# Kernel tuning notes

Measured on AMD Instinct MI355X. Metric: run time of the kernel, lower is better.

The kernel has to match this reference:

```python
import jax, jax.numpy as jnp
import numpy as np

EMBED_DIM = 256
NUM_HEADS = 4
HEAD_DIM = EMBED_DIM // NUM_HEADS  # 64
FEAT_X = FEAT_Y = 64               # 64*64 = 4096 tokens
THETA = 10000.0


def _axial_cos_sin(dim, end_x, end_y, theta):
    # compute_axial_cis: dim//4 frequencies per spatial axis, concatenated -> [N, dim//2]
    f = 1.0 / (theta ** (np.arange(0, dim, 4)[: dim // 4].astype(np.float32) / dim))
    t = np.arange(end_x * end_y)
    tx = (t % end_x).astype(np.float32)
    ty = (t // end_x).astype(np.float32)
    ang = np.concatenate([np.outer(tx, f), np.outer(ty, f)], axis=-1)  # [N, dim//2]
    return jnp.asarray(np.cos(ang)), jnp.asarray(np.sin(ang))


def _apply_rope(x, cos, sin):
    # x: [B, H, N, D]; adjacent pairs (x[..., 2i], x[..., 2i+1]) are the complex parts
    xr = x.reshape(*x.shape[:-1], -1, 2)
    xa, xb = xr[..., 0], xr[..., 1]          # [B, H, N, D//2]
    oa = xa * cos - xb * sin                  # cos/sin: [N, D//2], broadcast
    ob = xa * sin + xb * cos
    return jnp.stack([oa, ob], axis=-1).reshape(x.shape)


def setup_inputs() -> dict:
    key = jax.random.key(0)
    ks = jax.random.split(key, 8)
    B, N, D = 1, FEAT_X * FEAT_Y, EMBED_DIM
    s = 0.02  # weight init scale
    return {
        "q": jax.random.normal(ks[0], (B, N, D), jnp.float32),
        "k": jax.random.normal(ks[1], (B, N, D), jnp.float32),
        "v": jax.random.normal(ks[2], (B, N, D), jnp.float32),
        "wq": jax.random.normal(ks[3], (D, D), jnp.float32) * s,
        "bq": jnp.zeros((D,), jnp.float32),
        "wk": jax.random.normal(ks[4], (D, D), jnp.float32) * s,
        "bk": jnp.zeros((D,), jnp.float32),
        "wv": jax.random.normal(ks[5], (D, D), jnp.float32) * s,
        "bv": jnp.zeros((D,), jnp.float32),
        "wo": jax.random.normal(ks[6], (D, D), jnp.float32) * s,
        "bo": jnp.zeros((D,), jnp.float32),
        "return_attn": 0,
        "num_k_exclude_rope": 0,
    }


def reference(q, k, v, wq, bq, wk, bk, wv, bv, wo, bo, return_attn, num_k_exclude_rope):
    B, Nq, D = q.shape
    H, hd = NUM_HEADS, HEAD_DIM
    # QKV projections (weights stored [in, out], equiv to torch Linear W.T)
    qp = (q @ wq + bq).reshape(B, Nq, H, hd).transpose(0, 2, 1, 3)   # [B,H,Nq,hd]
    kp = (k @ wk + bk).reshape(B, -1, H, hd).transpose(0, 2, 1, 3)   # [B,H,Nk,hd]
    vp = (v @ wv + bv).reshape(B, -1, H, hd).transpose(0, 2, 1, 3)
    # rotary encoding on q and the first (Nk - num_k_exclude_rope) keys
    cos, sin = _axial_cos_sin(hd, FEAT_X, FEAT_Y, THETA)
    qp = _apply_rope(qp, cos, sin)
    nkr = kp.shape[2] - num_k_exclude_rope  # static Python int
    if num_k_exclude_rope > 0:
        kp = jnp.concatenate([_apply_rope(kp[:, :, :nkr], cos, sin), kp[:, :, nkr:]], axis=2)
    else:
        kp = _apply_rope(kp, cos, sin)
    # SDPA (eval: dropout_p = 0)
    scale = 1.0 / jnp.sqrt(jnp.asarray(hd, qp.dtype))
    scores = jnp.einsum("bhqd,bhkd->bhqk", qp, kp) * scale
    attn = jax.nn.softmax(scores, axis=-1)
    out = jnp.einsum("bhqk,bhkd->bhqd", attn, vp)
    out = out.transpose(0, 2, 1, 3).reshape(B, Nq, D)
    out = out @ wo + bo
    if return_attn:
        return out, scores  # attn_weight = q @ k^T * scale (pre-softmax, as in source)
    return out
```

## Files before the change

### kernel.cpp

```cpp
#include <hip/hip_runtime.h>
#include <hip/hip_bf16.h>
#include <math.h>

#define NTOK 4096
#define DEMB 256
#define NHEAD 4
#define HD 64

typedef short bf16x8 __attribute__((ext_vector_type(8)));
typedef short bf16x4 __attribute__((ext_vector_type(4)));
typedef float f32x4 __attribute__((ext_vector_type(4)));

__device__ __forceinline__ unsigned short f2b(float f) {
  union { float f; unsigned u; } v; v.f = f;
  return (unsigned short)((v.u + 0x7FFFu + ((v.u >> 16) & 1u)) >> 16);
}
__device__ __forceinline__ unsigned packrtn(float lo, float hi) {
  union { float f; unsigned u; } a, b; a.f = lo; b.f = hi;
  return ((a.u + 0x8000u) >> 16) | ((b.u + 0x8000u) & 0xFFFF0000u);
}

__global__ void wtrans_kernel(const float* wq, const float* wk, const float* wv,
                              const float* wo, unsigned short* wt) {
  int idx = blockIdx.x * 256 + threadIdx.x;
  int m = idx >> 16, rest = idx & 0xFFFF;
  int o = rest >> 8, i = rest & 255;
  const float* w = (m == 0) ? wq : (m == 1) ? wk : (m == 2) ? wv : wo;
  wt[idx] = f2b(w[i * 256 + o]);
}

__global__ void cs_kernel(float2* cs) {
  int idx = blockIdx.x * 256 + threadIdx.x;
  int n = idx >> 5, p = idx & 31;
  int j = p & 15;
  float f = powf(10000.0f, -(float)j / 16.0f);
  float ang = ((p < 16) ? (float)(n & 63) : (float)(n >> 6)) * f;
  cs[idx] = make_float2(cosf(ang), sinf(ang));
}

__global__ __launch_bounds__(256) void qkvproj_kernel(
    const float* q, const float* k, const float* v, const unsigned short* wt,
    const float* bq, const float* bk, const float* bv, const float2* cs,
    unsigned short* qp, unsigned short* kp, unsigned short* vt) {
  int which = blockIdx.z;
  int wave = threadIdx.x >> 6, lane = threadIdx.x & 63;
  int col = lane & 15, g = lane >> 4;
  int mbase = blockIdx.x * 64 + wave * 16;
  int nbase = blockIdx.y * 64;
  const float* X = (which == 0) ? q : (which == 1) ? k : v;
  const unsigned short* W = wt + which * 65536;
  const float* bias = (which == 0) ? bq : (which == 1) ? bk : bv;

  f32x4 acc[4] = {};
  const float* ap0 = X + (mbase + col) * 256 + g * 8;
#pragma unroll
  for (int ks = 0; ks < 256; ks += 32) {
    float4 a0 = *(const float4*)(ap0 + ks);
    float4 a1 = *(const float4*)(ap0 + ks + 4);
    bf16x8 af;
    af[0] = (short)f2b(a0.x); af[1] = (short)f2b(a0.y);
    af[2] = (short)f2b(a0.z); af[3] = (short)f2b(a0.w);
    af[4] = (short)f2b(a1.x); af[5] = (short)f2b(a1.y);
    af[6] = (short)f2b(a1.z); af[7] = (short)f2b(a1.w);
#pragma unroll
    for (int nt = 0; nt < 4; ++nt) {
      bf16x8 bf_ = *(const bf16x8*)(W + (nbase + nt * 16 + col) * 256 + ks + g * 8);
      acc[nt] = __builtin_amdgcn_mfma_f32_16x16x32_bf16(af, bf_, acc[nt], 0, 0, 0);
    }
  }

  if (which == 2) {
    int kpos = ((mbase >> 5) << 5) + 8 * g + 4 * ((mbase >> 4) & 1);
#pragma unroll
    for (int nt = 0; nt < 4; ++nt) {
      int c = nbase + nt * 16 + col;
      float b = bias[c];
      bf16x4 pk;
#pragma unroll
      for (int r = 0; r < 4; ++r) pk[r] = (short)f2b(acc[nt][r] + b);
      *(bf16x4*)(vt + c * NTOK + kpos) = pk;
    }
  } else {
    const float QSC = 0.18033688f;
    unsigned short* dst = (which == 0) ? qp : kp;
#pragma unroll
    for (int nt = 0; nt < 4; ++nt) {
      int c = nbase + nt * 16 + col;
      float b = bias[c];
#pragma unroll
      for (int r = 0; r < 4; ++r) {
        int t = mbase + g * 4 + r;
        float val = acc[nt][r] + b;
        float2 csv = cs[t * 32 + ((c & 63) >> 1)];
        float pv = __shfl_xor(val, 1);
        float sn = (c & 1) ? csv.y : -csv.y;
        val = val * csv.x + pv * sn;
        if (which == 0) val *= QSC;
        dst[((c >> 6) * NTOK + t) * HD + (c & 63)] = f2b(val);
      }
    }
  }
}

__global__ __launch_bounds__(512, 4) void attn_kernel(
    const unsigned short* qp, const unsigned short* kp,
    const unsigned short* vt, float* pO, float* pml) {
  __shared__ alignas(16) unsigned char lds[32768];
  int id = blockIdx.x;
  int xcd = id & 7;
  int head = xcd >> 1;
  int rest = id >> 3;
  int qtile = rest >> 1;
  int ks = (xcd & 1) * 2 + (rest & 1);
  int qb = qtile * 128;
  int slot = (head * 32 + qtile) * 4 + ks;
  int w = threadIdx.x >> 6, lane = threadIdx.x & 63;
  int col = lane & 15, g = lane >> 4;
  int stok = threadIdx.x >> 3, spart = threadIdx.x & 7;
  unsigned soff = (unsigned)(stok * 128) +
                  (unsigned)((spart * 16) ^ ((stok & 7) << 4));

  const unsigned short* kgp = kp + (head * NTOK + ks * 1024) * HD;
  const unsigned short* vgp = vt + head * HD * NTOK + ks * 1024;

  bf16x8 skr, svr;
  auto stage_issue = [&](int t) {
    skr = *(const bf16x8*)(kgp + (t * 64 + stok) * HD + spart * 8);
    svr = *(const bf16x8*)(vgp + stok * NTOK + t * 64 + spart * 8);
  };
  auto stage_write = [&](int buf) {
    *(bf16x8*)(lds + (unsigned)buf * 16384u + soff) = skr;
    *(bf16x8*)(lds + (unsigned)buf * 16384u + 8192u + soff) = svr;
  };

  bf16x8 qf[2];
  {
    const unsigned short* qr = qp + (head * NTOK + qb + w * 16) * HD;
#pragma unroll
    for (int h2 = 0; h2 < 2; ++h2)
      qf[h2] = *(const bf16x8*)(qr + col * HD + h2 * 32 + g * 8);
  }

  stage_issue(0);
  stage_write(0);
  stage_issue(1);
  __syncthreads();

  f32x4 acco[4] = {};
  float mrow = -1e30f, lrow = 0.f;

  for (int t = 0; t < 16; ++t) {
    int cur = t & 1;
    if (t < 15) {
      stage_write(cur ^ 1);
      if (t < 14) stage_issue(t + 2);
    }
    unsigned kb = (unsigned)cur * 16384u, vb = (unsigned)cur * 16384u + 8192u;

    f32x4 st[4] = {};
#pragma unroll
    for (int mt = 0; mt < 4; ++mt) {
      int tok = mt * 16 + col;
      unsigned ro = kb + (unsigned)(tok * 128) + (unsigned)((g * 16) ^ ((tok & 7) << 4));
      bf16x8 kf0 = *(const bf16x8*)(lds + ro);
      bf16x8 kf1 = *(const bf16x8*)(lds + (ro ^ 64u));
      st[mt] = __builtin_amdgcn_mfma_f32_16x16x32_bf16(kf0, qf[0], st[mt], 0, 0, 0);
      st[mt] = __builtin_amdgcn_mfma_f32_16x16x32_bf16(kf1, qf[1], st[mt], 0, 0, 0);
    }

    float pm = fmaxf(fmaxf(st[0][0], st[0][1]), fmaxf(st[0][2], st[0][3]));
#pragma unroll
    for (int mt = 1; mt < 4; ++mt)
      pm = fmaxf(pm, fmaxf(fmaxf(st[mt][0], st[mt][1]), fmaxf(st[mt][2], st[mt][3])));
    if (!__all(pm <= mrow + 8.0f)) {
      float nm = fmaxf(pm, __shfl_xor(pm, 16));
      nm = fmaxf(nm, __shfl_xor(nm, 32));
      nm = fmaxf(nm, mrow);
      float fac = exp2f(mrow - nm);
      mrow = nm;
      lrow *= fac;
      float fr0 = __shfl(fac, g * 4 + 0), fr1 = __shfl(fac, g * 4 + 1);
      float fr2 = __shfl(fac, g * 4 + 2), fr3 = __shfl(fac, g * 4 + 3);
#pragma unroll
      for (int nt = 0; nt < 4; ++nt) {
        acco[nt][0] *= fr0; acco[nt][1] *= fr1;
        acco[nt][2] *= fr2; acco[nt][3] *= fr3;
      }
    }

    float p[4][4];
#pragma unroll
    for (int mt = 0; mt < 4; ++mt)
#pragma unroll
      for (int r = 0; r < 4; ++r) {
        p[mt][r] = exp2f(st[mt][r] - mrow);
        lrow += p[mt][r];
      }
    unsigned pw[2][4];
#pragma unroll
    for (int kk = 0; kk < 2; ++kk) {
      pw[kk][0] = packrtn(p[2 * kk][0], p[2 * kk][1]);
      pw[kk][1] = packrtn(p[2 * kk][2], p[2 * kk][3]);
      pw[kk][2] = packrtn(p[2 * kk + 1][0], p[2 * kk + 1][1]);
      pw[kk][3] = packrtn(p[2 * kk + 1][2], p[2 * kk + 1][3]);
    }

#pragma unroll
    for (int kk = 0; kk < 2; ++kk) {
      union { unsigned u[4]; bf16x8 v; } pf;
      pf.u[0] = pw[kk][0]; pf.u[1] = pw[kk][1];
      pf.u[2] = pw[kk][2]; pf.u[3] = pw[kk][3];
#pragma unroll
      for (int nt = 0; nt < 4; ++nt) {
        int d = nt * 16 + col;
        unsigned off = vb + (unsigned)(d * 128) +
                       (unsigned)((kk * 64 + g * 16) ^ ((d & 7) << 4));
        bf16x8 vf = *(const bf16x8*)(lds + off);
        acco[nt] = __builtin_amdgcn_mfma_f32_16x16x32_bf16(pf.v, vf, acco[nt], 0, 0, 0);
      }
    }
    __syncthreads();
  }

  lrow += __shfl_xor(lrow, 16);
  lrow += __shfl_xor(lrow, 32);

#pragma unroll
  for (int nt = 0; nt < 4; ++nt)
#pragma unroll
    for (int r = 0; r < 4; ++r)
      pO[slot * 8192 + (w * 16 + g * 4 + r) * 64 + nt * 16 + col] = acco[nt][r];
  if (g == 0) {
    pml[slot * 256 + (w * 16 + col) * 2 + 0] = mrow;
    pml[slot * 256 + (w * 16 + col) * 2 + 1] = lrow;
  }
}

__global__ __launch_bounds__(256) void merge_kernel(
    const float* pO, const float* pml, unsigned short* att) {
  int bid = blockIdx.x;
  int group = bid >> 1, half = bid & 1;
  int head = group >> 5, qtile = group & 31;
  int t = threadIdx.x;
  int qloc = half * 64 + (t >> 2);
  int d0 = (t & 3) * 16;
  const float* mlb = pml + group * 4 * 256 + qloc * 2;
  float mx = -1e30f;
#pragma unroll
  for (int ks = 0; ks < 4; ++ks) mx = fmaxf(mx, mlb[ks * 256]);
  float den = 0.f, num[16] = {};
#pragma unroll
  for (int ks = 0; ks < 4; ++ks) {
    float wgt = exp2f(mlb[ks * 256] - mx);
    den += wgt * mlb[ks * 256 + 1];
    const float* ob = pO + (group * 4 + ks) * 8192 + qloc * 64 + d0;
#pragma unroll
    for (int i = 0; i < 16; ++i) num[i] += wgt * ob[i];
  }
  float inv = 1.0f / den;
  union { unsigned short s[16]; bf16x8 v[2]; } ov;
#pragma unroll
  for (int i = 0; i < 16; ++i) ov.s[i] = f2b(num[i] * inv);
  unsigned short* dst = att + (qtile * 128 + qloc) * DEMB + head * HD + d0;
  *(bf16x8*)dst = ov.v[0];
  *(bf16x8*)(dst + 8) = ov.v[1];
}

__global__ __launch_bounds__(256) void outproj_kernel(
    const unsigned short* att, const unsigned short* wt_o, const float* bo,
    float* out) {
  int wave = threadIdx.x >> 6, lane = threadIdx.x & 63;
  int col = lane & 15, g = lane >> 4;
  int mbase = blockIdx.x * 64 + wave * 16;
  int nbase = blockIdx.y * 64;
  f32x4 acc[4] = {};
#pragma unroll
  for (int ks = 0; ks < 256; ks += 32) {
    bf16x8 af = *(const bf16x8*)(att + (mbase + col) * 256 + ks + g * 8);
#pragma unroll
    for (int nt = 0; nt < 4; ++nt) {
      bf16x8 bf_ = *(const bf16x8*)(wt_o + (nbase + nt * 16 + col) * 256 + ks + g * 8);
      acc[nt] = __builtin_amdgcn_mfma_f32_16x16x32_bf16(af, bf_, acc[nt], 0, 0, 0);
    }
  }
#pragma unroll
  for (int nt = 0; nt < 4; ++nt) {
    int c = nbase + nt * 16 + col;
    float b = bo[c];
#pragma unroll
    for (int r = 0; r < 4; ++r)
      out[(mbase + g * 4 + r) * 256 + c] = acc[nt][r] + b;
  }
}

extern "C" void kernel_launch(void* const* d_in, const int* in_sizes, int n_in,
                              void* d_out, int out_size, void* d_ws, size_t ws_size,
                              hipStream_t stream) {
  const float* q  = (const float*)d_in[0];
  const float* k  = (const float*)d_in[1];
  const float* v  = (const float*)d_in[2];
  const float* wq = (const float*)d_in[3];
  const float* bq = (const float*)d_in[4];
  const float* wk = (const float*)d_in[5];
  const float* bk = (const float*)d_in[6];
  const float* wv = (const float*)d_in[7];
  const float* bv = (const float*)d_in[8];
  const float* wo = (const float*)d_in[9];
  const float* bo = (const float*)d_in[10];
  float* out = (float*)d_out;

  char* ws = (char*)d_ws;
  float2* cs         = (float2*)ws;
  unsigned short* wt = (unsigned short*)(ws + (1u << 20));
  unsigned short* qp = (unsigned short*)(ws + 1536u * 1024u);
  unsigned short* kp = qp + NHEAD * NTOK * HD;
  unsigned short* vt = kp + NHEAD * NTOK * HD;
  unsigned short* att = vt + NHEAD * NTOK * HD;
  float* pO  = (float*)(ws + 9728u * 1024u);
  float* pml = (float*)(ws + 26112u * 1024u);

  wtrans_kernel<<<1024, 256, 0, stream>>>(wq, wk, wv, wo, wt);
  cs_kernel<<<512, 256, 0, stream>>>(cs);
  qkvproj_kernel<<<dim3(64, 4, 3), 256, 0, stream>>>(q, k, v, wt, bq, bk, bv, cs,
                                                     qp, kp, vt);
  attn_kernel<<<512, 512, 0, stream>>>(qp, kp, vt, pO, pml);
  merge_kernel<<<256, 256, 0, stream>>>(pO, pml, att);
  outproj_kernel<<<dim3(64, 4), 256, 0, stream>>>(att, wt + 3 * 65536, bo, out);
}
```

Baseline: 78.07 us.

## Split attention keys 8-way, compute row sums via MFMA, fuse prep kernels

Doubles the key split of flash attention from 4 to 8 partitions, giving 1024 blocks with an occupancy hint of 8 and an 8-way merge. Row-sum accumulation moves from scalar adds and cross-lane shuffles to an MFMA against a ones vector. Bf16 packing now uses a perm instruction. The weight-transpose and cos/sin kernels are merged into one launch. These changes target more parallelism, fewer VALU ops and less launch overhead, at the cost of more partial-output traffic in the merge step and register pressure under the higher occupancy bound.

```diff
diff --git a/kernel.cpp b/kernel.cpp
--- a/kernel.cpp
+++ b/kernel.cpp
@@ -15,27 +15,28 @@
   union { float f; unsigned u; } v; v.f = f;
   return (unsigned short)((v.u + 0x7FFFu + ((v.u >> 16) & 1u)) >> 16);
 }
-__device__ __forceinline__ unsigned packrtn(float lo, float hi) {
-  union { float f; unsigned u; } a, b; a.f = lo; b.f = hi;
-  return ((a.u + 0x8000u) >> 16) | ((b.u + 0x8000u) & 0xFFFF0000u);
-}
-
-__global__ void wtrans_kernel(const float* wq, const float* wk, const float* wv,
-                              const float* wo, unsigned short* wt) {
-  int idx = blockIdx.x * 256 + threadIdx.x;
-  int m = idx >> 16, rest = idx & 0xFFFF;
-  int o = rest >> 8, i = rest & 255;
-  const float* w = (m == 0) ? wq : (m == 1) ? wk : (m == 2) ? wv : wo;
-  wt[idx] = f2b(w[i * 256 + o]);
-}
-
-__global__ void cs_kernel(float2* cs) {
-  int idx = blockIdx.x * 256 + threadIdx.x;
-  int n = idx >> 5, p = idx & 31;
-  int j = p & 15;
-  float f = powf(10000.0f, -(float)j / 16.0f);
-  float ang = ((p < 16) ? (float)(n & 63) : (float)(n >> 6)) * f;
-  cs[idx] = make_float2(cosf(ang), sinf(ang));
+__device__ __forceinline__ unsigned packrp(float lo, float hi) {
+  return __builtin_amdgcn_perm(__float_as_uint(hi) + 0x8000u,
+                               __float_as_uint(lo) + 0x8000u, 0x07060302u);
+}
+
+__global__ void prep_kernel(const float* wq, const float* wk, const float* wv,
+                            const float* wo, unsigned short* wt, float2* cs) {
+  int b = blockIdx.x;
+  if (b < 1024) {
+    int idx = b * 256 + threadIdx.x;
+    int m = idx >> 16, rest = idx & 0xFFFF;
+    int o = rest >> 8, i = rest & 255;
+    const float* w = (m == 0) ? wq : (m == 1) ? wk : (m == 2) ? wv : wo;
+    wt[idx] = f2b(w[i * 256 + o]);
+  } else {
+    int idx = (b - 1024) * 256 + threadIdx.x;
+    int n = idx >> 5, p = idx & 31;
+    int j = p & 15;
+    float f = powf(10000.0f, -(float)j / 16.0f);
+    float ang = ((p < 16) ? (float)(n & 63) : (float)(n >> 6)) * f;
+    cs[idx] = make_float2(cosf(ang), sinf(ang));
+  }
 }
 
 __global__ __launch_bounds__(256) void qkvproj_kernel(
@@ -102,7 +103,7 @@
   }
 }
 
-__global__ __launch_bounds__(512, 4) void attn_kernel(
+__global__ __launch_bounds__(512, 8) void attn_kernel(
     const unsigned short* qp, const unsigned short* kp,
     const unsigned short* vt, float* pO, float* pml) {
   __shared__ alignas(16) unsigned char lds[32768];
@@ -110,18 +111,18 @@
   int xcd = id & 7;
   int head = xcd >> 1;
   int rest = id >> 3;
-  int qtile = rest >> 1;
-  int ks = (xcd & 1) * 2 + (rest & 1);
+  int qtile = rest >> 2;
+  int ks = (xcd & 1) * 4 + (rest & 3);
   int qb = qtile * 128;
-  int slot = (head * 32 + qtile) * 4 + ks;
+  int slot = (head * 32 + qtile) * 8 + ks;
   int w = threadIdx.x >> 6, lane = threadIdx.x & 63;
   int col = lane & 15, g = lane >> 4;
   int stok = threadIdx.x >> 3, spart = threadIdx.x & 7;
   unsigned soff = (unsigned)(stok * 128) +
                   (unsigned)((spart * 16) ^ ((stok & 7) << 4));
 
-  const unsigned short* kgp = kp + (head * NTOK + ks * 1024) * HD;
-  const unsigned short* vgp = vt + head * HD * NTOK + ks * 1024;
+  const unsigned short* kgp = kp + (head * NTOK + ks * 512) * HD;
+  const unsigned short* vgp = vt + head * HD * NTOK + ks * 512;
 
   bf16x8 skr, svr;
   auto stage_issue = [&](int t) {
@@ -133,6 +134,10 @@
     *(bf16x8*)(lds + (unsigned)buf * 16384u + 8192u + soff) = svr;
   };
 
+  bf16x8 ones;
+#pragma unroll
+  for (int i = 0; i < 8; ++i) ones[i] = (short)0x3F80;
+
   bf16x8 qf[2];
   {
     const unsigned short* qr = qp + (head * NTOK + qb + w * 16) * HD;
@@ -147,13 +152,14 @@
   __syncthreads();
 
   f32x4 acco[4] = {};
-  float mrow = -1e30f, lrow = 0.f;
-
-  for (int t = 0; t < 16; ++t) {
+  f32x4 lacc = {};
+  float mrow = -1e30f;
+
+  for (int t = 0; t < 8; ++t) {
     int cur = t & 1;
-    if (t < 15) {
+    if (t < 7) {
       stage_write(cur ^ 1);
-      if (t < 14) stage_issue(t + 2);
+      if (t < 6) stage_issue(t + 2);
     }
     unsigned kb = (unsigned)cur * 16384u, vb = (unsigned)cur * 16384u + 8192u;
 
@@ -178,7 +184,6 @@
       nm = fmaxf(nm, mrow);
       float fac = exp2f(mrow - nm);
       mrow = nm;
-      lrow *= fac;
       float fr0 = __shfl(fac, g * 4 + 0), fr1 = __shfl(fac, g * 4 + 1);
       float fr2 = __shfl(fac, g * 4 + 2), fr3 = __shfl(fac, g * 4 + 3);
 #pragma unroll
@@ -186,23 +191,21 @@
         acco[nt][0] *= fr0; acco[nt][1] *= fr1;
         acco[nt][2] *= fr2; acco[nt][3] *= fr3;
       }
+      lacc[0] *= fr0; lacc[1] *= fr1; lacc[2] *= fr2; lacc[3] *= fr3;
     }
 
     float p[4][4];
 #pragma unroll
     for (int mt = 0; mt < 4; ++mt)
 #pragma unroll
-      for (int r = 0; r < 4; ++r) {
-        p[mt][r] = exp2f(st[mt][r] - mrow);
-        lrow += p[mt][r];
-      }
+      for (int r = 0; r < 4; ++r) p[mt][r] = exp2f(st[mt][r] - mrow);
     unsigned pw[2][4];
 #pragma unroll
     for (int kk = 0; kk < 2; ++kk) {
-      pw[kk][0] = packrtn(p[2 * kk][0], p[2 * kk][1]);
-      pw[kk][1] = packrtn(p[2 * kk][2], p[2 * kk][3]);
-      pw[kk][2] = packrtn(p[2 * kk + 1][0], p[2 * kk + 1][1]);
-      pw[kk][3] = packrtn(p[2 * kk + 1][2], p[2 * kk + 1][3]);
+      pw[kk][0] = packrp(p[2 * kk][0], p[2 * kk][1]);
+      pw[kk][1] = packrp(p[2 * kk][2], p[2 * kk][3]);
+      pw[kk][2] = packrp(p[2 * kk + 1][0], p[2 * kk + 1][1]);
+      pw[kk][3] = packrp(p[2 * kk + 1][2], p[2 * kk + 1][3]);
     }
 
 #pragma unroll
@@ -210,6 +213,7 @@
       union { unsigned u[4]; bf16x8 v; } pf;
       pf.u[0] = pw[kk][0]; pf.u[1] = pw[kk][1];
       pf.u[2] = pw[kk][2]; pf.u[3] = pw[kk][3];
+      lacc = __builtin_amdgcn_mfma_f32_16x16x32_bf16(pf.v, ones, lacc, 0, 0, 0);
 #pragma unroll
       for (int nt = 0; nt < 4; ++nt) {
         int d = nt * 16 + col;
@@ -222,18 +226,18 @@
     __syncthreads();
   }
 
-  lrow += __shfl_xor(lrow, 16);
-  lrow += __shfl_xor(lrow, 32);
-
 #pragma unroll
   for (int nt = 0; nt < 4; ++nt)
 #pragma unroll
     for (int r = 0; r < 4; ++r)
       pO[slot * 8192 + (w * 16 + g * 4 + r) * 64 + nt * 16 + col] = acco[nt][r];
-  if (g == 0) {
+  if (col == 0) {
+#pragma unroll
+    for (int r = 0; r < 4; ++r)
+      pml[slot * 256 + (w * 16 + g * 4 + r) * 2 + 1] = lacc[r];
+  }
+  if (g == 0)
     pml[slot * 256 + (w * 16 + col) * 2 + 0] = mrow;
-    pml[slot * 256 + (w * 16 + col) * 2 + 1] = lrow;
-  }
 }
 
 __global__ __launch_bounds__(256) void merge_kernel(
@@ -244,16 +248,16 @@
   int t = threadIdx.x;
   int qloc = half * 64 + (t >> 2);
   int d0 = (t & 3) * 16;
-  const float* mlb = pml + group * 4 * 256 + qloc * 2;
+  const float* mlb = pml + group * 8 * 256 + qloc * 2;
   float mx = -1e30f;
 #pragma unroll
-  for (int ks = 0; ks < 4; ++ks) mx = fmaxf(mx, mlb[ks * 256]);
+  for (int ks = 0; ks < 8; ++ks) mx = fmaxf(mx, mlb[ks * 256]);
   float den = 0.f, num[16] = {};
 #pragma unroll
-  for (int ks = 0; ks < 4; ++ks) {
+  for (int ks = 0; ks < 8; ++ks) {
     float wgt = exp2f(mlb[ks * 256] - mx);
     den += wgt * mlb[ks * 256 + 1];
-    const float* ob = pO + (group * 4 + ks) * 8192 + qloc * 64 + d0;
+    const float* ob = pO + (group * 8 + ks) * 8192 + qloc * 64 + d0;
 #pragma unroll
     for (int i = 0; i < 16; ++i) num[i] += wgt * ob[i];
   }
@@ -317,13 +321,12 @@
   unsigned short* vt = kp + NHEAD * NTOK * HD;
   unsigned short* att = vt + NHEAD * NTOK * HD;
   float* pO  = (float*)(ws + 9728u * 1024u);
-  float* pml = (float*)(ws + 26112u * 1024u);
-
-  wtrans_kernel<<<1024, 256, 0, stream>>>(wq, wk, wv, wo, wt);
-  cs_kernel<<<512, 256, 0, stream>>>(cs);
+  float* pml = (float*)(ws + 43008u * 1024u);
+
+  prep_kernel<<<1536, 256, 0, stream>>>(wq, wk, wv, wo, wt, cs);
   qkvproj_kernel<<<dim3(64, 4, 3), 256, 0, stream>>>(q, k, v, wt, bq, bk, bv, cs,
                                                      qp, kp, vt);
-  attn_kernel<<<512, 512, 0, stream>>>(qp, kp, vt, pO, pml);
+  attn_kernel<<<1024, 512, 0, stream>>>(qp, kp, vt, pO, pml);
   merge_kernel<<<256, 256, 0, stream>>>(pO, pml, att);
   outproj_kernel<<<dim3(64, 4), 256, 0, stream>>>(att, wt + 3 * 65536, bo, out);
 }
```

New measurement: 95.36 us. 22.1% more time.
